# Kernel optimization log

Hardware: AMD Instinct MI355X
Metric: run time of the kernel (lower is better)

Reference implementation:

```python
import jax, jax.numpy as jnp
import numpy as np

POLY_Q = 2.0  # normalizer='poly_2'
N_HEADS = 12
LN_EPS = 1e-5  # torch nn.LayerNorm default


def poly_norm(x, q=POLY_Q):
    # Newton solve for c such that sum_k 1/(-x-c)^q == 1, row-wise (last axis).
    c = jnp.min(-x, axis=-1, keepdims=True) - 1.0  # ensures -x - c >= 1
    for _ in range(6):
        base = -x - c
        poly_sum = jnp.sum(base ** (-q), axis=-1, keepdims=True)
        poly_sum_der = q * jnp.sum(base ** (-(q + 1.0)), axis=-1, keepdims=True)
        c = c - (poly_sum - 1.0) / (poly_sum_der + 1e-8)
    return (-x - c) ** (-q)


def layer_norm(x, g, b, eps=LN_EPS):
    m = jnp.mean(x, axis=-1, keepdims=True)
    v = jnp.mean((x - m) ** 2, axis=-1, keepdims=True)
    return (x - m) * jax.lax.rsqrt(v + eps) * g + b


def setup_inputs() -> dict:
    key = jax.random.key(0)
    B, S, D, M = 2, 1024, 768, 3072
    ks = jax.random.split(key, 8)
    sd = 1.0 / np.sqrt(D)
    sm = 1.0 / np.sqrt(M)
    return {
        "x": jax.random.normal(ks[0], (B, S, D), dtype=jnp.float32),
        "ln1_g": jnp.ones((D,), jnp.float32),
        "ln1_b": jnp.zeros((D,), jnp.float32),
        "wq": jax.random.normal(ks[1], (D, D), jnp.float32) * sd,
        "bq": jnp.zeros((D,), jnp.float32),
        "wk": jax.random.normal(ks[2], (D, D), jnp.float32) * sd,
        "bk": jnp.zeros((D,), jnp.float32),
        "wv": jax.random.normal(ks[3], (D, D), jnp.float32) * sd,
        "bv": jnp.zeros((D,), jnp.float32),
        "wo": jax.random.normal(ks[4], (D, D), jnp.float32) * sd,
        "bo": jnp.zeros((D,), jnp.float32),
        "ln2_g": jnp.ones((D,), jnp.float32),
        "ln2_b": jnp.zeros((D,), jnp.float32),
        "w1": jax.random.normal(ks[5], (D, M), jnp.float32) * sd,
        "b1": jnp.zeros((M,), jnp.float32),
        "w2": jax.random.normal(ks[6], (M, D), jnp.float32) * sm,
        "b2": jnp.zeros((D,), jnp.float32),
    }


def reference(x, ln1_g, ln1_b, wq, bq, wk, bk, wv, bv, wo, bo,
              ln2_g, ln2_b, w1, b1, w2, b2):
    B, S, D = x.shape
    H = N_HEADS
    Dh = D // H
    # --- pre-LN self-attention with poly normalizer ---
    y = layer_norm(x, ln1_g, ln1_b)
    q = (y @ wq + bq).reshape(B, S, H, Dh) / jnp.sqrt(jnp.float32(Dh))
    k = (y @ wk + bk).reshape(B, S, H, Dh)
    v = (y @ wv + bv).reshape(B, S, H, Dh)
    scores = jnp.einsum('bqhd,bkhd->bhqk', q, k)  # [B,H,S,S]
    attn_w = poly_norm(scores)
    attn = jnp.einsum('bhqk,bkhd->bqhd', attn_w, v).reshape(B, S, D)
    x1 = x + attn @ wo + bo  # residual 1
    # --- MLP block ---
    y2 = layer_norm(x1, ln2_g, ln2_b)
    h = jax.nn.gelu(y2 @ w1 + b1, approximate=False)  # torch GELU = exact erf
    out = x1 + h @ w2 + b2  # residual 2
    return out
```

## Files before the change

kernel.cpp:

```cpp
#include <hip/hip_runtime.h>

#define DEV __device__ __forceinline__

typedef unsigned short u16;
typedef __attribute__((ext_vector_type(8))) short bf16x8;
typedef __attribute__((ext_vector_type(4))) float f32x4;
typedef __attribute__((ext_vector_type(4))) unsigned int u32x4;

DEV u16 f2bf(float f) {
  union { float f; unsigned u; } un; un.f = f;
  unsigned r = un.u + 0x7fffu + ((un.u >> 16) & 1u);
  return (u16)(r >> 16);
}

DEV void gload16(const void* g, void* l) {
  __builtin_amdgcn_global_load_lds((const __attribute__((address_space(1))) void*)g,
                                   (__attribute__((address_space(3))) void*)l, 16, 0, 0);
}

template <int N>
DEV void vm_wait() { asm volatile("s_waitcnt vmcnt(%0)" :: "n"(N) : "memory"); }

DEV float blk_sum(float v, volatile float* sb) {
#pragma unroll
  for (int o = 32; o; o >>= 1) v += __shfl_xor(v, o);
  __syncthreads();
  if ((threadIdx.x & 63) == 0) sb[threadIdx.x >> 6] = v;
  __syncthreads();
  return sb[0] + sb[1] + sb[2] + sb[3];
}

__global__ __launch_bounds__(256) void ln_kernel(const float* __restrict__ x,
                                                 const float* __restrict__ g,
                                                 const float* __restrict__ b,
                                                 u16* __restrict__ y) {
  __shared__ float sb[4];
  const size_t row = blockIdx.x;
  const float* xr = x + row * 768;
  const int t = threadIdx.x;
  float v0 = xr[t], v1 = xr[t + 256], v2 = xr[t + 512];
  float mean = blk_sum(v0 + v1 + v2, sb) * (1.0f / 768.0f);
  float d0 = v0 - mean, d1 = v1 - mean, d2 = v2 - mean;
  float var = blk_sum(d0 * d0 + d1 * d1 + d2 * d2, sb) * (1.0f / 768.0f);
  float inv = rsqrtf(var + 1e-5f);
  u16* yr = y + row * 768;
  yr[t]       = f2bf(d0 * inv * g[t]       + b[t]);
  yr[t + 256] = f2bf(d1 * inv * g[t + 256] + b[t + 256]);
  yr[t + 512] = f2bf(d2 * inv * g[t + 512] + b[t + 512]);
}

__global__ __launch_bounds__(256) void wt_transpose(const float* __restrict__ in,
                                                    u16* __restrict__ out, int K, int N) {
  __shared__ float tile[32][33];
  const int tx = threadIdx.x & 31, ty = threadIdx.x >> 5;
  const int n0 = blockIdx.x * 32, k0 = blockIdx.y * 32;
#pragma unroll
  for (int i = 0; i < 4; i++)
    tile[ty + 8 * i][tx] = in[(size_t)(k0 + ty + 8 * i) * N + n0 + tx];
  __syncthreads();
#pragma unroll
  for (int i = 0; i < 4; i++)
    out[(size_t)(n0 + ty + 8 * i) * K + k0 + tx] = f2bf(tile[tx][ty + 8 * i]);
}

__global__ __launch_bounds__(256) void v_transpose(const u16* __restrict__ qkv,
                                                   u16* __restrict__ vT) {
  __shared__ u16 tile[32][33];
  const int tx = threadIdx.x & 31, ty = threadIdx.x >> 5;
  const int z = blockIdx.z, b = z / 12, h = z % 12;
  const int s0 = blockIdx.x * 32, d0 = blockIdx.y * 32;
#pragma unroll
  for (int i = 0; i < 4; i++)
    tile[ty + 8 * i][tx] =
        qkv[(size_t)(b * 1024 + s0 + ty + 8 * i) * 2304 + 1536 + h * 64 + d0 + tx];
  __syncthreads();
#pragma unroll
  for (int i = 0; i < 4; i++)
    vT[(size_t)(z * 64 + d0 + ty + 8 * i) * 1024 + s0 + tx] = tile[tx][ty + 8 * i];
}

__global__ __launch_bounds__(512) void fused_attn(const u16* __restrict__ qkv,
                                                  const u16* __restrict__ vT,
                                                  u16* __restrict__ attn) {
  __shared__ __align__(16) u16 wlds[16 * 1024];
  __shared__ float sp2[16][8], sp3[16][8];
  __shared__ float cl[16];

  const int tid = threadIdx.x;
  const int w = tid >> 6, l = tid & 63;
  const int g = l >> 4, lr = l & 15;
  const int bh = blockIdx.y, b = bh / 12, h = bh % 12;
  const int q0 = blockIdx.x * 16;

  const u16* qrow = qkv + (size_t)(b * 1024 + q0 + lr) * 2304 + h * 64;
  const u16* krow = qkv + (size_t)(b * 1024 + w * 128 + lr) * 2304 + 768 + h * 64;

  bf16x8 af[2];
  af[0] = *(const bf16x8*)(qrow + g * 8);
  af[1] = *(const bf16x8*)(qrow + 32 + g * 8);

  f32x4 acc[8];
#pragma unroll
  for (int n = 0; n < 8; n++) acc[n] = (f32x4){0.f, 0.f, 0.f, 0.f};

#pragma unroll
  for (int n = 0; n < 8; n++) {
    bf16x8 b0 = *(const bf16x8*)(krow + n * 16 * 2304 + g * 8);
    bf16x8 b1 = *(const bf16x8*)(krow + n * 16 * 2304 + 32 + g * 8);
    acc[n] = __builtin_amdgcn_mfma_f32_16x16x32_bf16(af[0], b0, acc[n], 0, 0, 0);
    acc[n] = __builtin_amdgcn_mfma_f32_16x16x32_bf16(af[1], b1, acc[n], 0, 0, 0);
  }

  float m4[4];
#pragma unroll
  for (int r = 0; r < 4; r++) {
    float v = acc[0][r];
#pragma unroll
    for (int n = 1; n < 8; n++) v = fmaxf(v, acc[n][r]);
    m4[r] = v;
  }
#pragma unroll
  for (int o = 1; o < 16; o <<= 1)
#pragma unroll
    for (int r = 0; r < 4; r++) m4[r] = fmaxf(m4[r], __shfl_xor(m4[r], o));
#pragma unroll
  for (int j = 0; j < 4; j++)
    if (lr == j) sp2[g * 4 + j][w] = m4[j];
  __syncthreads();
  if (tid < 16) {
    float v = sp2[tid][0];
#pragma unroll
    for (int j = 1; j < 8; j++) v = fmaxf(v, sp2[tid][j]);
    cl[tid] = -v - 1.0f;
  }
  __syncthreads();

  float c[4];
#pragma unroll
  for (int r = 0; r < 4; r++) c[r] = cl[g * 4 + r];

#pragma unroll 1
  for (int it = 0; it < 6; it++) {
    float s2[4], s3[4];
#pragma unroll
    for (int r = 0; r < 4; r++) { s2[r] = 0.f; s3[r] = 0.f; }
#pragma unroll
    for (int n = 0; n < 8; n++)
#pragma unroll
      for (int r = 0; r < 4; r++) {
        float rr = __builtin_amdgcn_rcpf(-acc[n][r] - c[r]);
        float r2 = rr * rr;
        s2[r] += r2;
        s3[r] = fmaf(r2, rr, s3[r]);
      }
#pragma unroll
    for (int o = 1; o < 16; o <<= 1)
#pragma unroll
      for (int r = 0; r < 4; r++) {
        s2[r] += __shfl_xor(s2[r], o);
        s3[r] += __shfl_xor(s3[r], o);
      }
#pragma unroll
    for (int j = 0; j < 4; j++)
      if (lr == j) {
        sp2[g * 4 + j][w] = s2[j];
        sp3[g * 4 + j][w] = s3[j];
      }
    __syncthreads();
    if (tid < 16) {
      float S2 = 0.f, S3 = 0.f;
#pragma unroll
      for (int j = 0; j < 8; j++) { S2 += sp2[tid][j]; S3 += sp3[tid][j]; }
      cl[tid] -= (S2 - 1.0f) * __builtin_amdgcn_rcpf(2.0f * S3 + 1e-8f);
    }
    __syncthreads();
#pragma unroll
    for (int r = 0; r < 4; r++) c[r] = cl[g * 4 + r];
  }

#pragma unroll
  for (int n = 0; n < 8; n++)
#pragma unroll
    for (int r = 0; r < 4; r++) {
      float rr = __builtin_amdgcn_rcpf(-acc[n][r] - c[r]);
      int row = g * 4 + r;
      int col = w * 128 + n * 16 + lr;
      unsigned off = (unsigned)(row * 2048 + col * 2);
      off ^= (unsigned)(row & 7) << 4;
      *(u16*)((char*)wlds + off) = f2bf(rr * rr);
    }
  __syncthreads();

  if (w < 4) {
    const int nf = w;
    const u16* vrow = vT + (size_t)(bh * 64 + nf * 16 + lr) * 1024;
    const unsigned swz = (unsigned)(lr & 7) << 4;
    const unsigned abase = (unsigned)(lr * 2048);
    f32x4 oacc = (f32x4){0.f, 0.f, 0.f, 0.f};
#pragma unroll
    for (int ks = 0; ks < 32; ks++) {
      bf16x8 afr = *(const bf16x8*)((const char*)wlds +
                                    ((abase + (unsigned)(ks * 64 + g * 16)) ^ swz));
      bf16x8 bfr = *(const bf16x8*)(vrow + ks * 32 + g * 8);
      oacc = __builtin_amdgcn_mfma_f32_16x16x32_bf16(afr, bfr, oacc, 0, 0, 0);
    }
    u16* orow = attn + (size_t)(b * 1024 + q0 + g * 4) * 768 + h * 64 + nf * 16 + lr;
#pragma unroll
    for (int r = 0; r < 4; r++) orow[(size_t)r * 768] = f2bf(oacc[r]);
  }
}

__global__ __launch_bounds__(256) void splitk_reduce(const float* __restrict__ p,
                                                     const float* __restrict__ bias,
                                                     const float* __restrict__ res,
                                                     float* __restrict__ out) {
  const size_t S = 2048ull * 768;
  size_t i = ((size_t)blockIdx.x * 256 + threadIdx.x) * 4;
  f32x4 v = *(const f32x4*)&p[i];
  v += *(const f32x4*)&p[i + S];
  v += *(const f32x4*)&p[i + 2 * S];
  v += *(const f32x4*)&p[i + 3 * S];
  int col = (int)(i % 768);
  v += *(const f32x4*)&bias[col];
  v += *(const f32x4*)&res[i];
  *(f32x4*)&out[i] = v;
}

template <int BM, int WN, int EPI>
__global__ __launch_bounds__(256) void gemm_bt(
    const u16* __restrict__ A, int lda, long long sAb, long long sAh,
    const u16* __restrict__ B0, const u16* __restrict__ B1, const u16* __restrict__ B2,
    int ldb, long long sBb, long long sBh,
    void* __restrict__ Cv, int ldc, long long sCb, long long sCh,
    const float* __restrict__ bias0, const float* __restrict__ bias1,
    const float* __restrict__ bias2, const float* __restrict__ res, int K) {
  constexpr int WCOL = (BM == 128) ? 2 : 4;
  constexpr int BN = WCOL * WN * 16;
  constexpr int NA = BM / 64;
  constexpr int NB = BN / 64;
  constexpr int LT = NA + NB;
  __shared__ __align__(16) u16 lds_a[3][BM * 32];
  __shared__ __align__(16) u16 lds_b[3][BN * 32];

  const int zb = blockIdx.z / 12, zh = blockIdx.z % 12;
  A += zb * sAb + zh * sAh;

  const int colbase = blockIdx.y * BN;
  const u16* B = B0;
  const float* bias = bias0;
  int biasoff = 0;
  float qscale = 1.0f;
  if (EPI == 0) {
    int sel = colbase / 768;
    B = (sel == 0) ? B0 : ((sel == 1) ? B1 : B2);
    bias = (sel == 0) ? bias0 : ((sel == 1) ? bias1 : bias2);
    biasoff = sel * 768;
    qscale = (sel == 0) ? 0.125f : 1.0f;
  }
  B += zb * sBb + zh * sBh;

  const int tid = threadIdx.x;
  const size_t ldab = (size_t)lda * 2, ldbb = (size_t)ldb * 2;
  const char* Abase = (const char*)(A + (size_t)blockIdx.x * BM * lda);
  const char* Bbase = (const char*)(B + (size_t)(colbase - biasoff) * ldb);

  const char* ap[NA];
  const char* bp[NB];
#pragma unroll
  for (int j = 0; j < NA; j++) {
    int lin = (j * 256 + tid) * 16;
    ap[j] = Abase + (size_t)(lin >> 6) * ldab + (lin & 63);
  }
#pragma unroll
  for (int j = 0; j < NB; j++) {
    int lin = (j * 256 + tid) * 16;
    bp[j] = Bbase + (size_t)(lin >> 6) * ldbb + (lin & 63);
  }

  auto stage = [&](int buf) {
#pragma unroll
    for (int j = 0; j < NA; j++) {
      gload16(ap[j], (char*)&lds_a[buf][0] + (j * 256 + tid) * 16);
      ap[j] += 64;
    }
#pragma unroll
    for (int j = 0; j < NB; j++) {
      gload16(bp[j], (char*)&lds_b[buf][0] + (j * 256 + tid) * 16);
      bp[j] += 64;
    }
  };

  f32x4 acc[4][WN];
#pragma unroll
  for (int m = 0; m < 4; m++)
#pragma unroll
    for (int n = 0; n < WN; n++) acc[m][n] = (f32x4){0.f, 0.f, 0.f, 0.f};

  const int w = tid >> 6, l = tid & 63;
  const int wm = (BM == 128) ? (w >> 1) : 0;
  const int wn = (BM == 128) ? (w & 1) : w;
  const int lr = l & 15, kg = l >> 4;

  const int nt = K / 32;
  stage(0);
  if (nt > 1) stage(1);

  for (int t = 0; t < nt; ++t) {
    const int buf = t % 3;
    if (t + 2 < nt) {
      stage((t + 2) % 3);
      vm_wait<2 * LT>();
    } else if (t + 1 < nt) {
      vm_wait<LT>();
    } else {
      vm_wait<0>();
    }
    __builtin_amdgcn_sched_barrier(0);
    __builtin_amdgcn_s_barrier();
    __builtin_amdgcn_sched_barrier(0);

    bf16x8 af[4], bfr[WN];
#pragma unroll
    for (int m = 0; m < 4; m++)
      af[m] = *(const bf16x8*)&lds_a[buf][(wm * 64 + m * 16 + lr) * 32 + kg * 8];
#pragma unroll
    for (int n = 0; n < WN; n++)
      bfr[n] = *(const bf16x8*)&lds_b[buf][(wn * WN * 16 + n * 16 + lr) * 32 + kg * 8];
#pragma unroll
    for (int m = 0; m < 4; m++)
#pragma unroll
      for (int n = 0; n < WN; n++)
        acc[m][n] = __builtin_amdgcn_mfma_f32_16x16x32_bf16(af[m], bfr[n], acc[m][n], 0, 0, 0);

    __builtin_amdgcn_sched_barrier(0);
    __builtin_amdgcn_s_barrier();
    __builtin_amdgcn_sched_barrier(0);
  }

  const int row0 = blockIdx.x * BM + ((BM == 128) ? wm * 64 : 0) + kg * 4;
  const int colb = colbase + wn * WN * 16;
  float* Cf = (float*)Cv + (size_t)zb * sCb + (size_t)zh * sCh;
  u16* Cu = (u16*)Cv + (size_t)zb * sCb + (size_t)zh * sCh;
#pragma unroll
  for (int m = 0; m < 4; m++) {
#pragma unroll
    for (int n = 0; n < WN; n++) {
#pragma unroll
      for (int r = 0; r < 4; r++) {
        int row = row0 + m * 16 + r;
        int col = colb + n * 16 + lr;
        size_t idx = (size_t)row * ldc + col;
        float v = acc[m][n][r];
        if (EPI == 0) {
          Cu[idx] = f2bf((v + bias[col - biasoff]) * qscale);
        } else if (EPI == 1) {
          Cf[idx] = v;
        } else if (EPI == 2) {
          Cu[idx] = f2bf(v);
        } else if (EPI == 3) {
          Cf[idx] = v + bias[col] + res[idx];
        } else {
          v += bias[col];
          Cu[idx] = f2bf(0.5f * v * (1.0f + erff(v * 0.70710678118654752f)));
        }
      }
    }
  }
}

extern "C" void kernel_launch(void* const* d_in, const int* in_sizes, int n_in,
                              void* d_out, int out_size, void* d_ws, size_t ws_size,
                              hipStream_t stream) {
  const float* x     = (const float*)d_in[0];
  const float* ln1_g = (const float*)d_in[1];
  const float* ln1_b = (const float*)d_in[2];
  const float* wq    = (const float*)d_in[3];
  const float* bq    = (const float*)d_in[4];
  const float* wk    = (const float*)d_in[5];
  const float* bk    = (const float*)d_in[6];
  const float* wv    = (const float*)d_in[7];
  const float* bv    = (const float*)d_in[8];
  const float* wo    = (const float*)d_in[9];
  const float* bo    = (const float*)d_in[10];
  const float* ln2_g = (const float*)d_in[11];
  const float* ln2_b = (const float*)d_in[12];
  const float* w1    = (const float*)d_in[13];
  const float* b1    = (const float*)d_in[14];
  const float* w2    = (const float*)d_in[15];
  const float* b2    = (const float*)d_in[16];
  float* out = (float*)d_out;

  char* p = (char*)d_ws;
  auto alloc = [&](size_t n) { char* r = p; p += (n + 255) & ~(size_t)255; return r; };
  u16*   qkv    = (u16*)  alloc(2048ull * 2304 * 2);
  u16*   y1     = (u16*)  alloc(2048ull * 768 * 2);
  u16*   vT     = (u16*)  alloc(24ull * 64 * 1024 * 2);
  u16*   attn   = (u16*)  alloc(2048ull * 768 * 2);
  float* x1     = (float*)alloc(2048ull * 768 * 4);
  u16*   y2     = (u16*)  alloc(2048ull * 768 * 2);
  u16*   hbuf   = (u16*)  alloc(2048ull * 3072 * 2);
  float* pbuf   = (float*)alloc(4ull * 2048 * 768 * 4);
  u16*   wq_t   = (u16*)  alloc(768ull * 768 * 2);
  u16*   wk_t   = (u16*)  alloc(768ull * 768 * 2);
  u16*   wv_t   = (u16*)  alloc(768ull * 768 * 2);
  u16*   wo_t   = (u16*)  alloc(768ull * 768 * 2);
  u16*   w1_t   = (u16*)  alloc(3072ull * 768 * 2);
  u16*   w2_t   = (u16*)  alloc(768ull * 3072 * 2);
  (void)in_sizes; (void)n_in; (void)out_size; (void)ws_size;

  wt_transpose<<<dim3(24, 24), 256, 0, stream>>>(wq, wq_t, 768, 768);
  wt_transpose<<<dim3(24, 24), 256, 0, stream>>>(wk, wk_t, 768, 768);
  wt_transpose<<<dim3(24, 24), 256, 0, stream>>>(wv, wv_t, 768, 768);
  wt_transpose<<<dim3(24, 24), 256, 0, stream>>>(wo, wo_t, 768, 768);
  wt_transpose<<<dim3(96, 24), 256, 0, stream>>>(w1, w1_t, 768, 3072);
  wt_transpose<<<dim3(24, 96), 256, 0, stream>>>(w2, w2_t, 3072, 768);

  ln_kernel<<<2048, 256, 0, stream>>>(x, ln1_g, ln1_b, y1);

  gemm_bt<128, 4, 0><<<dim3(16, 18, 1), 256, 0, stream>>>(
      y1, 768, 0, 0, wq_t, wk_t, wv_t, 768, 0, 0, qkv, 2304, 0, 0, bq, bk, bv, nullptr, 768);

  v_transpose<<<dim3(32, 2, 24), 256, 0, stream>>>(qkv, vT);

  fused_attn<<<dim3(64, 24), 512, 0, stream>>>(qkv, vT, attn);

  gemm_bt<64, 2, 3><<<dim3(32, 6, 1), 256, 0, stream>>>(
      attn, 768, 0, 0, wo_t, nullptr, nullptr, 768, 0, 0, x1, 768, 0, 0,
      bo, nullptr, nullptr, x, 768);

  ln_kernel<<<2048, 256, 0, stream>>>(x1, ln2_g, ln2_b, y2);

  gemm_bt<128, 4, 4><<<dim3(16, 24, 1), 256, 0, stream>>>(
      y2, 768, 0, 0, w1_t, nullptr, nullptr, 768, 0, 0, hbuf, 3072, 0, 0,
      b1, nullptr, nullptr, nullptr, 768);

  gemm_bt<64, 2, 1><<<dim3(32, 6, 4), 256, 0, stream>>>(
      hbuf, 3072, 0, 768LL, w2_t, nullptr, nullptr, 3072, 0, 768LL,
      pbuf, 768, 0, 1572864LL, nullptr, nullptr, nullptr, nullptr, 768);

  splitk_reduce<<<1536, 256, 0, stream>>>(pbuf, b2, x1, out);
}
```

Before: 191.6 us.

## Transpose scores through LDS so each row's Newton solve stays within one wave

Raw attention scores are now written to LDS as bf16, then reread so that 32 lanes of a single wave own each query row. The max and the six Newton iterations use only wave-level shuffles, which removes the cross-wave shared-memory reductions and the roughly 14 block-wide barriers. The cost is that scores are rounded to bf16 before the normaliser runs, which changes numerics and could hurt accuracy. Each thread also holds 32 floats in registers, and an extra LDS round trip is added.

```diff
diff --git a/kernel.cpp b/kernel.cpp
--- a/kernel.cpp
+++ b/kernel.cpp
@@ -83,8 +83,6 @@
                                                   const u16* __restrict__ vT,
                                                   u16* __restrict__ attn) {
   __shared__ __align__(16) u16 wlds[16 * 1024];
-  __shared__ float sp2[16][8], sp3[16][8];
-  __shared__ float cl[16];
 
   const int tid = threadIdx.x;
   const int w = tid >> 6, l = tid & 63;
@@ -111,84 +109,71 @@
     acc[n] = __builtin_amdgcn_mfma_f32_16x16x32_bf16(af[1], b1, acc[n], 0, 0, 0);
   }
 
-  float m4[4];
-#pragma unroll
-  for (int r = 0; r < 4; r++) {
-    float v = acc[0][r];
-#pragma unroll
-    for (int n = 1; n < 8; n++) v = fmaxf(v, acc[n][r]);
-    m4[r] = v;
-  }
-#pragma unroll
-  for (int o = 1; o < 16; o <<= 1)
-#pragma unroll
-    for (int r = 0; r < 4; r++) m4[r] = fmaxf(m4[r], __shfl_xor(m4[r], o));
-#pragma unroll
-  for (int j = 0; j < 4; j++)
-    if (lr == j) sp2[g * 4 + j][w] = m4[j];
-  __syncthreads();
-  if (tid < 16) {
-    float v = sp2[tid][0];
-#pragma unroll
-    for (int j = 1; j < 8; j++) v = fmaxf(v, sp2[tid][j]);
-    cl[tid] = -v - 1.0f;
-  }
-  __syncthreads();
-
-  float c[4];
-#pragma unroll
-  for (int r = 0; r < 4; r++) c[r] = cl[g * 4 + r];
-
-#pragma unroll 1
-  for (int it = 0; it < 6; it++) {
-    float s2[4], s3[4];
-#pragma unroll
-    for (int r = 0; r < 4; r++) { s2[r] = 0.f; s3[r] = 0.f; }
-#pragma unroll
-    for (int n = 0; n < 8; n++)
-#pragma unroll
-      for (int r = 0; r < 4; r++) {
-        float rr = __builtin_amdgcn_rcpf(-acc[n][r] - c[r]);
-        float r2 = rr * rr;
-        s2[r] += r2;
-        s3[r] = fmaf(r2, rr, s3[r]);
-      }
-#pragma unroll
-    for (int o = 1; o < 16; o <<= 1)
-#pragma unroll
-      for (int r = 0; r < 4; r++) {
-        s2[r] += __shfl_xor(s2[r], o);
-        s3[r] += __shfl_xor(s3[r], o);
-      }
-#pragma unroll
-    for (int j = 0; j < 4; j++)
-      if (lr == j) {
-        sp2[g * 4 + j][w] = s2[j];
-        sp3[g * 4 + j][w] = s3[j];
-      }
-    __syncthreads();
-    if (tid < 16) {
-      float S2 = 0.f, S3 = 0.f;
-#pragma unroll
-      for (int j = 0; j < 8; j++) { S2 += sp2[tid][j]; S3 += sp3[tid][j]; }
-      cl[tid] -= (S2 - 1.0f) * __builtin_amdgcn_rcpf(2.0f * S3 + 1e-8f);
-    }
-    __syncthreads();
-#pragma unroll
-    for (int r = 0; r < 4; r++) c[r] = cl[g * 4 + r];
-  }
-
 #pragma unroll
   for (int n = 0; n < 8; n++)
 #pragma unroll
     for (int r = 0; r < 4; r++) {
-      float rr = __builtin_amdgcn_rcpf(-acc[n][r] - c[r]);
       int row = g * 4 + r;
       int col = w * 128 + n * 16 + lr;
       unsigned off = (unsigned)(row * 2048 + col * 2);
       off ^= (unsigned)(row & 7) << 4;
-      *(u16*)((char*)wlds + off) = f2bf(rr * rr);
-    }
+      *(u16*)((char*)wlds + off) = f2bf(acc[n][r]);
+    }
+  __syncthreads();
+
+  const int crow = tid >> 5, l32 = tid & 31;
+  const unsigned cswz = (unsigned)(crow & 7) << 4;
+  const unsigned cbase = (unsigned)(crow * 2048 + l32 * 64);
+  float xs[32];
+#pragma unroll
+  for (int j = 0; j < 4; j++) {
+    u32x4 raw = *(const u32x4*)((const char*)wlds + ((cbase + j * 16u) ^ cswz));
+#pragma unroll
+    for (int e = 0; e < 4; e++) {
+      union { unsigned u; float f; } lo, hi;
+      lo.u = raw[e] << 16;
+      hi.u = raw[e] & 0xffff0000u;
+      xs[j * 8 + e * 2] = lo.f;
+      xs[j * 8 + e * 2 + 1] = hi.f;
+    }
+  }
+
+  float mx = xs[0];
+#pragma unroll
+  for (int i = 1; i < 32; i++) mx = fmaxf(mx, xs[i]);
+#pragma unroll
+  for (int o = 1; o < 32; o <<= 1) mx = fmaxf(mx, __shfl_xor(mx, o));
+  float c = -mx - 1.0f;
+
+#pragma unroll 1
+  for (int it = 0; it < 6; it++) {
+    float s2 = 0.f, s3 = 0.f;
+#pragma unroll
+    for (int i = 0; i < 32; i++) {
+      float rr = __builtin_amdgcn_rcpf(-(xs[i] + c));
+      float r2 = rr * rr;
+      s2 += r2;
+      s3 = fmaf(r2, rr, s3);
+    }
+#pragma unroll
+    for (int o = 1; o < 32; o <<= 1) {
+      s2 += __shfl_xor(s2, o);
+      s3 += __shfl_xor(s3, o);
+    }
+    c -= (s2 - 1.0f) * __builtin_amdgcn_rcpf(2.0f * s3 + 1e-8f);
+  }
+
+#pragma unroll
+  for (int j = 0; j < 4; j++) {
+    u32x4 outv;
+#pragma unroll
+    for (int e = 0; e < 4; e++) {
+      float r0 = __builtin_amdgcn_rcpf(-(xs[j * 8 + e * 2] + c));
+      float r1 = __builtin_amdgcn_rcpf(-(xs[j * 8 + e * 2 + 1] + c));
+      outv[e] = (unsigned)f2bf(r0 * r0) | ((unsigned)f2bf(r1 * r1) << 16);
+    }
+    *(u32x4*)((char*)wlds + ((cbase + j * 16u) ^ cswz)) = outv;
+  }
   __syncthreads();
 
   if (w < 4) {
```

After: 182.7 us. 1.05x faster.
